# Optimization experiments

Hardware: AMD Instinct MI355X
Metric: run time of the kernel (lower is better)

The kernel has to match this reference:

```python
import jax, jax.numpy as jnp
import numpy as np
from jax import lax


def setup_inputs() -> dict:
    key = jax.random.key(0)
    k1, k2, k3, k4 = jax.random.split(key, 4)
    N, T = 4096, 64          # num_nodes, tokens per node
    V, H, L = 30000, 256, 2  # vocab, hidden size, LSTM layers
    data = jax.random.randint(k1, (N, T), 0, V, dtype=jnp.int64)
    embed = jax.random.uniform(k2, (V, H), jnp.float32, -0.1, 0.1)
    Wx = jax.random.normal(k3, (L, H, 4 * H), jnp.float32) * 0.05
    Wh = jax.random.normal(k4, (L, H, 4 * H), jnp.float32) * 0.05
    b = jnp.zeros((L, 4 * H), jnp.float32)
    return {"data": data, "embed": embed, "Wx": Wx, "Wh": Wh, "b": b}


def _stacked_lstm_last(tok, Wx, Wh, b):
    # tok: [N, T, H]; Wx/Wh: [L, H, 4H]; b: [L, 4H]
    L, H = Wx.shape[0], Wx.shape[1]
    N = tok.shape[0]
    xs = jnp.swapaxes(tok, 0, 1)  # [T, N, H] -- scan over time, batched over nodes
    c0 = jnp.zeros((L, N, H), tok.dtype)
    h0 = jnp.zeros((L, N, H), tok.dtype)

    def step(carry, x_t):
        c, h = carry
        inp = x_t
        new_c, new_h = [], []
        for l in range(L):  # small fixed layer loop
            z = inp @ Wx[l] + h[l] @ Wh[l] + b[l]  # [N, 4H]
            i, f, g, o = jnp.split(z, 4, axis=-1)   # flax gate order i, f, g, o
            i, f, o = jax.nn.sigmoid(i), jax.nn.sigmoid(f), jax.nn.sigmoid(o)
            g = jnp.tanh(g)
            cl = f * c[l] + i * g
            hl = o * jnp.tanh(cl)
            new_c.append(cl)
            new_h.append(hl)
            inp = hl  # top layer output feeds next layer
        return (jnp.stack(new_c), jnp.stack(new_h)), None

    (_, hF), _ = lax.scan(step, (c0, h0), xs)
    # result[-1] in the original is the top-layer output at the final step,
    # which equals the final top-layer hidden state.
    return hF[-1]  # [N, H]


def reference(data, embed, Wx, Wh, b):
    tok = embed[data]  # [N, T, H] embedding lookup
    return _stacked_lstm_last(tok, Wx, Wh, b)
```

## Files before the change

### kernel.cpp

```cpp
#include <hip/hip_runtime.h>
#include <hip/hip_bf16.h>

#define TT 64
#define HH 256
#define GG 1024

typedef _Float16 f16;
typedef __attribute__((ext_vector_type(8))) _Float16 f16x8;
typedef __attribute__((ext_vector_type(4))) _Float16 f16x4;
typedef __attribute__((ext_vector_type(4))) float f32x4;

__device__ __forceinline__ float sig_(float x) {
    return 1.0f / (1.0f + __expf(-x));
}
__device__ __forceinline__ float tanh_(float x) {
    x = fminf(fmaxf(x, -15.0f), 15.0f);
    float e = __expf(-2.0f * x);
    return (1.0f - e) / (1.0f + e);
}

__global__ void pack_weights(const float* __restrict__ Wx, const float* __restrict__ Wh,
                             f16* __restrict__ Wp) {
    int t = blockIdx.x * 256 + threadIdx.x;
    int lane = t & 63;
    int nt = (t >> 6) & 63;
    int kk = (t >> 12) & 15;
    int l = t >> 16;
    int n = nt * 16 + (lane & 15);
    int kbase = kk * 32 + 8 * (lane >> 4);
    const float* src = (kbase < 256) ? (Wx + (size_t)l * HH * GG + (size_t)kbase * GG + n)
                                     : (Wh + (size_t)l * HH * GG + (size_t)(kbase - 256) * GG + n);
    f16x8 v;
#pragma unroll
    for (int j = 0; j < 8; ++j) v[j] = (f16)src[(size_t)j * GG];
    *(f16x8*)(Wp + (size_t)t * 8) = v;
}

__global__ __launch_bounds__(512) void embw_gemm(
    const float* __restrict__ embed, const float* __restrict__ bias,
    const f16* __restrict__ Wp, f16* __restrict__ embW, int vocab)
{
    __shared__ f16 a_lds[32 * HH];
    const int tid = threadIdx.x;
    const int lane = tid & 63;
    const int w = tid >> 6;
    const int arow = lane & 15;
    const int g4 = lane >> 4;
    const int r0 = blockIdx.x * 32;

#pragma unroll
    for (int i = 0; i < 4; ++i) {
        int chunk = tid + i * 512;
        int row = chunk >> 6;
        int c4 = chunk & 63;
        int grow = r0 + row; if (grow >= vocab) grow = vocab - 1;
        float4 v = *(const float4*)(embed + (size_t)grow * HH + c4 * 4);
        int idx = row * HH + ((c4 * 4) ^ ((row & 7) << 3));
        *(f16x4*)&a_lds[idx] = (f16x4){(f16)v.x, (f16)v.y, (f16)v.z, (f16)v.w};
    }
    __syncthreads();

    float breg[8];
#pragma unroll
    for (int tt = 0; tt < 8; ++tt) breg[tt] = bias[(w * 8 + tt) * 16 + arow];

    f32x4 acc[2][8];
#pragma unroll
    for (int mt = 0; mt < 2; ++mt)
#pragma unroll
        for (int tt = 0; tt < 8; ++tt)
            acc[mt][tt] = (f32x4){breg[tt], breg[tt], breg[tt], breg[tt]};

    const f16* wl = Wp + (size_t)lane * 8;
#pragma unroll 2
    for (int kk = 0; kk < 8; ++kk) {
        int sw = (kk * 32 + g4 * 8) ^ ((arow & 7) << 3);
        f16x8 a0 = *(const f16x8*)&a_lds[arow * HH + sw];
        f16x8 a1 = *(const f16x8*)&a_lds[(arow + 16) * HH + sw];
        const f16* wkk = wl + (size_t)kk * 64 * 64 * 8;
#pragma unroll
        for (int tt = 0; tt < 8; ++tt) {
            f16x8 b = *(const f16x8*)(wkk + (size_t)(w * 8 + tt) * 64 * 8);
            acc[0][tt] = __builtin_amdgcn_mfma_f32_16x16x32_f16(a0, b, acc[0][tt], 0, 0, 0);
            acc[1][tt] = __builtin_amdgcn_mfma_f32_16x16x32_f16(a1, b, acc[1][tt], 0, 0, 0);
        }
    }

#pragma unroll
    for (int mt = 0; mt < 2; ++mt)
#pragma unroll
        for (int tt = 0; tt < 8; ++tt)
#pragma unroll
            for (int r = 0; r < 4; ++r) {
                int row = r0 + mt * 16 + g4 * 4 + r;
                if (row < vocab) {
                    int col = (w * 8 + tt) * 16 + arow;
                    embW[(size_t)row * GG + col] = (f16)acc[mt][tt][r];
                }
            }
}

#define NB2 16
#define LDZ 1032
#define LDH 264

__global__ __launch_bounds__(512, 2) void lstm_rec2(
    const int* __restrict__ data, const float* __restrict__ bias,
    const f16* __restrict__ embW, const f16* __restrict__ Wp,
    float* __restrict__ out)
{
    __shared__ f16 zx[NB2 * LDZ];
    __shared__ f16 h0s[NB2 * LDH];
    __shared__ f16 h1s[NB2 * LDH];

    const int tid = threadIdx.x;
    const int lane = tid & 63;
    const int w = tid >> 6;
    const int arow = lane & 15;
    const int g4 = lane >> 4;
    const int n0 = blockIdx.x * NB2;

    for (int i = tid; i < NB2 * LDH; i += 512) { h0s[i] = (f16)0; h1s[i] = (f16)0; }

    float breg1[8];
#pragma unroll
    for (int tt = 0; tt < 8; ++tt) {
        int col = (tt >> 1) * 256 + w * 32 + (tt & 1) * 16 + arow;
        breg1[tt] = bias[GG + col];
    }

    float c0[8], c1[8];
#pragma unroll
    for (int i = 0; i < 8; ++i) { c0[i] = 0.0f; c1[i] = 0.0f; }

    __syncthreads();

    const f16* wl0 = Wp + (size_t)8 * 64 * 64 * 8 + (size_t)lane * 8;
    const f16* wl1 = Wp + (size_t)16 * 64 * 64 * 8 + (size_t)lane * 8;

    for (int t = 0; t < TT; ++t) {
        {
            int n = tid >> 5;
            int cg = (tid & 31) * 32;
            int row = data[(n0 + n) * TT + t];
            const f16* src = embW + (size_t)row * GG + cg;
            f16x8 v0 = *(const f16x8*)src;
            f16x8 v1 = *(const f16x8*)(src + 8);
            f16x8 v2 = *(const f16x8*)(src + 16);
            f16x8 v3 = *(const f16x8*)(src + 24);
            f16* dst = &zx[n * LDZ + cg];
            *(f16x8*)dst = v0;
            *(f16x8*)(dst + 8) = v1;
            *(f16x8*)(dst + 16) = v2;
            *(f16x8*)(dst + 24) = v3;
        }
        __syncthreads();

        f32x4 acc[8];
#pragma unroll
        for (int tt = 0; tt < 8; ++tt) {
            int col = (tt >> 1) * 256 + w * 32 + (tt & 1) * 16 + arow;
#pragma unroll
            for (int r = 0; r < 4; ++r)
                acc[tt][r] = (float)zx[(g4 * 4 + r) * LDZ + col];
        }

#pragma unroll 2
        for (int kk = 0; kk < 8; ++kk) {
            int k0 = kk * 32 + 8 * g4;
            f16x8 a0 = *(const f16x8*)&h0s[arow * LDH + k0];
            const f16* wkk = wl0 + (size_t)kk * 64 * 64 * 8;
#pragma unroll
            for (int tt = 0; tt < 8; ++tt) {
                int nt = (tt >> 1) * 16 + w * 2 + (tt & 1);
                f16x8 b = *(const f16x8*)(wkk + (size_t)nt * 64 * 8);
                acc[tt] = __builtin_amdgcn_mfma_f32_16x16x32_f16(a0, b, acc[tt], 0, 0, 0);
            }
        }
        __syncthreads();

#pragma unroll
        for (int sub = 0; sub < 2; ++sub)
#pragma unroll
            for (int r = 0; r < 4; ++r) {
                int node = g4 * 4 + r;
                float i_ = sig_(acc[0 + sub][r]);
                float f_ = sig_(acc[2 + sub][r]);
                float g_ = tanh_(acc[4 + sub][r]);
                float o_ = sig_(acc[6 + sub][r]);
                int ci = sub * 4 + r;
                float c = fmaf(f_, c0[ci], i_ * g_);
                c0[ci] = c;
                int u = w * 32 + sub * 16 + arow;
                h0s[node * LDH + u] = (f16)(o_ * tanh_(c));
            }
        __syncthreads();

        f32x4 acc1[8];
#pragma unroll
        for (int tt = 0; tt < 8; ++tt)
            acc1[tt] = (f32x4){breg1[tt], breg1[tt], breg1[tt], breg1[tt]};

#pragma unroll 2
        for (int kk = 0; kk < 16; ++kk) {
            const f16* asrc = (kk < 8) ? h0s : h1s;
            int k0 = (kk & 7) * 32 + 8 * g4;
            f16x8 a0 = *(const f16x8*)&asrc[arow * LDH + k0];
            const f16* wkk = wl1 + (size_t)kk * 64 * 64 * 8;
#pragma unroll
            for (int tt = 0; tt < 8; ++tt) {
                int nt = (tt >> 1) * 16 + w * 2 + (tt & 1);
                f16x8 b = *(const f16x8*)(wkk + (size_t)nt * 64 * 8);
                acc1[tt] = __builtin_amdgcn_mfma_f32_16x16x32_f16(a0, b, acc1[tt], 0, 0, 0);
            }
        }
        __syncthreads();

#pragma unroll
        for (int sub = 0; sub < 2; ++sub)
#pragma unroll
            for (int r = 0; r < 4; ++r) {
                int node = g4 * 4 + r;
                float i_ = sig_(acc1[0 + sub][r]);
                float f_ = sig_(acc1[2 + sub][r]);
                float g_ = tanh_(acc1[4 + sub][r]);
                float o_ = sig_(acc1[6 + sub][r]);
                int ci = sub * 4 + r;
                float c = fmaf(f_, c1[ci], i_ * g_);
                c1[ci] = c;
                int u = w * 32 + sub * 16 + arow;
                h1s[node * LDH + u] = (f16)(o_ * tanh_(c));
            }
    }
    __syncthreads();

    for (int i = tid; i < NB2 * HH; i += 512) {
        int n = i >> 8, k = i & 255;
        out[(size_t)(n0 + n) * HH + k] = (float)h1s[n * LDH + k];
    }
}

__global__ void convert_embed(const float* __restrict__ e, f16* __restrict__ o, int n8) {
    int i = blockIdx.x * 256 + threadIdx.x;
    if (i >= n8) return;
    size_t p = (size_t)i * 8;
    float4 a = *(const float4*)(e + p);
    float4 b = *(const float4*)(e + p + 4);
    f16x8 v = { (f16)a.x, (f16)a.y, (f16)a.z, (f16)a.w,
                (f16)b.x, (f16)b.y, (f16)b.z, (f16)b.w };
    *(f16x8*)(o + p) = v;
}

#define FB 32
#define FTH 512
#define FLD 264
__device__ __forceinline__ void fb_layer_step(
    const f16 (*bx)[FLD], f16 (*bh)[FLD], const f16* __restrict__ wlayer,
    const float* breg_l, float* c_l, int lane, int w)
{
    f32x4 acc[2][8];
#pragma unroll
    for (int mt = 0; mt < 2; ++mt)
#pragma unroll
        for (int tt = 0; tt < 8; ++tt) {
            float b = breg_l[tt];
            acc[mt][tt] = (f32x4){b, b, b, b};
        }
    const int arow = lane & 15;
    const int koff = 8 * (lane >> 4);
    const f16* wl = wlayer + (size_t)lane * 8;
#pragma unroll 2
    for (int kk = 0; kk < 16; ++kk) {
        int k0 = (kk & 7) * 32 + koff;
        const f16(*src)[FLD] = (kk < 8) ? bx : (const f16(*)[FLD])bh;
        f16x8 a0 = *(const f16x8*)&src[arow][k0];
        f16x8 a1 = *(const f16x8*)&src[arow + 16][k0];
        const f16* wkk = wl + (size_t)kk * 64 * 64 * 8;
#pragma unroll
        for (int tt = 0; tt < 8; ++tt) {
            int nt = (tt >> 1) * 16 + w * 2 + (tt & 1);
            f16x8 b = *(const f16x8*)(wkk + (size_t)nt * 64 * 8);
            acc[0][tt] = __builtin_amdgcn_mfma_f32_16x16x32_f16(a0, b, acc[0][tt], 0, 0, 0);
            acc[1][tt] = __builtin_amdgcn_mfma_f32_16x16x32_f16(a1, b, acc[1][tt], 0, 0, 0);
        }
    }
    __syncthreads();
#pragma unroll
    for (int mt = 0; mt < 2; ++mt)
#pragma unroll
        for (int sub = 0; sub < 2; ++sub) {
            f32x4 iv = acc[mt][0 + sub], fv = acc[mt][2 + sub];
            f32x4 gv = acc[mt][4 + sub], ov = acc[mt][6 + sub];
#pragma unroll
            for (int r = 0; r < 4; ++r) {
                float i_ = sig_(iv[r]), f_ = sig_(fv[r]), g_ = tanh_(gv[r]), o_ = sig_(ov[r]);
                int ci = mt * 8 + sub * 4 + r;
                float c = fmaf(f_, c_l[ci], i_ * g_);
                c_l[ci] = c;
                int node = mt * 16 + (lane >> 4) * 4 + r;
                int unit = w * 32 + sub * 16 + (lane & 15);
                bh[node][unit] = (f16)(o_ * tanh_(c));
            }
        }
    __syncthreads();
}

__global__ __launch_bounds__(FTH, 2) void lstm_mfma_fb(
    const int* __restrict__ data, const float* __restrict__ bias,
    const f16* __restrict__ emb, const f16* __restrict__ Wp,
    float* __restrict__ out, int vocab)
{
    __shared__ f16 x_lds[FB][FLD];
    __shared__ f16 h0_lds[FB][FLD];
    __shared__ f16 h1_lds[FB][FLD];
    const int tid = threadIdx.x;
    const int lane = tid & 63;
    const int w = tid >> 6;
    const int n0 = blockIdx.x * FB;
    for (int i = tid; i < FB * FLD; i += FTH) {
        (&h0_lds[0][0])[i] = (f16)0.0f; (&h1_lds[0][0])[i] = (f16)0.0f;
    }
    float breg[2][8];
#pragma unroll
    for (int l = 0; l < 2; ++l)
#pragma unroll
        for (int tt = 0; tt < 8; ++tt) {
            int col = (tt >> 1) * 256 + w * 32 + (tt & 1) * 16 + (lane & 15);
            breg[l][tt] = bias[l * GG + col];
        }
    float cst[2][16];
#pragma unroll
    for (int i = 0; i < 32; ++i) (&cst[0][0])[i] = 0.0f;
    __syncthreads();
    const f16* Wp0 = Wp;
    const f16* Wp1 = Wp + (size_t)16 * 64 * 64 * 8;
    for (int t = 0; t < TT; ++t) {
        {
            int n = tid >> 4;
            int cg = (tid & 15) * 16;
            int row = data[(n0 + n) * TT + t];
            row = min(max(row, 0), vocab - 1);
            const f16* src = emb + (size_t)row * HH + cg;
            *(f16x8*)&x_lds[n][cg] = *(const f16x8*)src;
            *(f16x8*)&x_lds[n][cg + 8] = *(const f16x8*)(src + 8);
        }
        __syncthreads();
        fb_layer_step(x_lds, h0_lds, Wp0, breg[0], cst[0], lane, w);
        fb_layer_step((const f16(*)[FLD])h0_lds, h1_lds, Wp1, breg[1], cst[1], lane, w);
    }
    for (int i = tid; i < FB * HH; i += FTH) {
        int n = i >> 8, k = i & 255;
        out[(size_t)(n0 + n) * HH + k] = (float)h1_lds[n][k];
    }
}

extern "C" void kernel_launch(void* const* d_in, const int* in_sizes, int n_in,
                              void* d_out, int out_size, void* d_ws, size_t ws_size,
                              hipStream_t stream) {
    const int* data = (const int*)d_in[0];
    const float* embed = (const float*)d_in[1];
    const float* Wx = (const float*)d_in[2];
    const float* Wh = (const float*)d_in[3];
    const float* bias = (const float*)d_in[4];
    float* out = (float*)d_out;
    const int vocab = in_sizes[1] / HH;
    const int nNodes = in_sizes[0] / TT;

    const size_t wp_bytes = (size_t)2 * 16 * 64 * 64 * 8 * 2;
    const size_t embw_bytes = (size_t)vocab * GG * 2;
    const size_t emb16_bytes = (size_t)vocab * HH * 2;

    if (ws_size >= embw_bytes + wp_bytes) {
        f16* embW = (f16*)d_ws;
        f16* Wp = (f16*)((char*)d_ws + embw_bytes);
        pack_weights<<<dim3(512), dim3(256), 0, stream>>>(Wx, Wh, Wp);
        embw_gemm<<<dim3((vocab + 31) / 32), dim3(512), 0, stream>>>(embed, bias, Wp, embW, vocab);
        lstm_rec2<<<dim3(nNodes / NB2), dim3(512), 0, stream>>>(data, bias, embW, Wp, out);
        return;
    }
    f16* emb_h = (f16*)d_ws;
    f16* Wp = (f16*)((char*)d_ws + emb16_bytes);
    int n8 = in_sizes[1] / 8;
    convert_embed<<<dim3((n8 + 255) / 256), dim3(256), 0, stream>>>(embed, emb_h, n8);
    pack_weights<<<dim3(512), dim3(256), 0, stream>>>(Wx, Wh, Wp);
    lstm_mfma_fb<<<dim3(nNodes / FB), dim3(FTH), 0, stream>>>(data, bias, emb_h, Wp, out, vocab);
}
```

Measured before the change: 1.295 ms.

## Process 32 nodes per block in recurrent LSTM kernel and use fast exp2/rcp activations

Doubles the nodes per block in lstm_rec2 from 16 to 32, so each weight fragment loaded from global memory feeds two MFMAs (two M-tiles) instead of one. This halves the weight traffic per node for the recurrent matmuls. In exchange it uses more registers and shared memory and drops occupancy to one block per CU, with half as many blocks in the grid. The sigmoid and tanh helpers also switch to hardware exp2 and rcp intrinsics without clamping, while the fallback kernel keeps the precise versions.

```diff
diff --git a/kernel.cpp b/kernel.cpp
--- a/kernel.cpp
+++ b/kernel.cpp
@@ -10,10 +10,15 @@
 typedef __attribute__((ext_vector_type(4))) _Float16 f16x4;
 typedef __attribute__((ext_vector_type(4))) float f32x4;
 
+__device__ __forceinline__ float exp2_(float x) { return __builtin_amdgcn_exp2f(x); }
 __device__ __forceinline__ float sig_(float x) {
-    return 1.0f / (1.0f + __expf(-x));
+    return __builtin_amdgcn_rcpf(1.0f + exp2_(-1.44269504f * x));
 }
 __device__ __forceinline__ float tanh_(float x) {
+    return 1.0f - 2.0f * __builtin_amdgcn_rcpf(1.0f + exp2_(2.88539008f * x));
+}
+__device__ __forceinline__ float sigp_(float x) { return 1.0f / (1.0f + __expf(-x)); }
+__device__ __forceinline__ float tanhp_(float x) {
     x = fminf(fmaxf(x, -15.0f), 15.0f);
     float e = __expf(-2.0f * x);
     return (1.0f - e) / (1.0f + e);
@@ -100,11 +105,11 @@
             }
 }
 
-#define NB2 16
+#define NB2 32
 #define LDZ 1032
 #define LDH 264
 
-__global__ __launch_bounds__(512, 2) void lstm_rec2(
+__global__ __launch_bounds__(512, 1) void lstm_rec2(
     const int* __restrict__ data, const float* __restrict__ bias,
     const f16* __restrict__ embW, const f16* __restrict__ Wp,
     float* __restrict__ out)
@@ -120,6 +125,10 @@
     const int g4 = lane >> 4;
     const int n0 = blockIdx.x * NB2;
 
+    const int sn = tid >> 4;
+    const int scg = (tid & 15) * 64;
+    const int srow_base = (n0 + sn) * TT;
+
     for (int i = tid; i < NB2 * LDH; i += 512) { h0s[i] = (f16)0; h1s[i] = (f16)0; }
 
     float breg1[8];
@@ -129,108 +138,112 @@
         breg1[tt] = bias[GG + col];
     }
 
-    float c0[8], c1[8];
-#pragma unroll
-    for (int i = 0; i < 8; ++i) { c0[i] = 0.0f; c1[i] = 0.0f; }
-
-    __syncthreads();
+    float c0[16], c1[16];
+#pragma unroll
+    for (int i = 0; i < 16; ++i) { c0[i] = 0.0f; c1[i] = 0.0f; }
 
     const f16* wl0 = Wp + (size_t)8 * 64 * 64 * 8 + (size_t)lane * 8;
     const f16* wl1 = Wp + (size_t)16 * 64 * 64 * 8 + (size_t)lane * 8;
 
+#pragma unroll 1
     for (int t = 0; t < TT; ++t) {
         {
-            int n = tid >> 5;
-            int cg = (tid & 31) * 32;
-            int row = data[(n0 + n) * TT + t];
-            const f16* src = embW + (size_t)row * GG + cg;
-            f16x8 v0 = *(const f16x8*)src;
-            f16x8 v1 = *(const f16x8*)(src + 8);
-            f16x8 v2 = *(const f16x8*)(src + 16);
-            f16x8 v3 = *(const f16x8*)(src + 24);
-            f16* dst = &zx[n * LDZ + cg];
-            *(f16x8*)dst = v0;
-            *(f16x8*)(dst + 8) = v1;
-            *(f16x8*)(dst + 16) = v2;
-            *(f16x8*)(dst + 24) = v3;
+            int row = data[srow_base + t];
+            const f16* src = embW + (size_t)row * GG + scg;
+            f16* dst = &zx[sn * LDZ + scg];
+#pragma unroll
+            for (int j = 0; j < 8; ++j)
+                *(f16x8*)(dst + j * 8) = *(const f16x8*)(src + j * 8);
         }
         __syncthreads();
 
-        f32x4 acc[8];
-#pragma unroll
-        for (int tt = 0; tt < 8; ++tt) {
-            int col = (tt >> 1) * 256 + w * 32 + (tt & 1) * 16 + arow;
-#pragma unroll
-            for (int r = 0; r < 4; ++r)
-                acc[tt][r] = (float)zx[(g4 * 4 + r) * LDZ + col];
-        }
+        f32x4 acc[2][8];
+#pragma unroll
+        for (int mt = 0; mt < 2; ++mt)
+#pragma unroll
+            for (int tt = 0; tt < 8; ++tt) {
+                int col = (tt >> 1) * 256 + w * 32 + (tt & 1) * 16 + arow;
+#pragma unroll
+                for (int r = 0; r < 4; ++r)
+                    acc[mt][tt][r] = (float)zx[(mt * 16 + g4 * 4 + r) * LDZ + col];
+            }
 
 #pragma unroll 2
         for (int kk = 0; kk < 8; ++kk) {
             int k0 = kk * 32 + 8 * g4;
             f16x8 a0 = *(const f16x8*)&h0s[arow * LDH + k0];
+            f16x8 a1 = *(const f16x8*)&h0s[(arow + 16) * LDH + k0];
             const f16* wkk = wl0 + (size_t)kk * 64 * 64 * 8;
 #pragma unroll
             for (int tt = 0; tt < 8; ++tt) {
                 int nt = (tt >> 1) * 16 + w * 2 + (tt & 1);
                 f16x8 b = *(const f16x8*)(wkk + (size_t)nt * 64 * 8);
-                acc[tt] = __builtin_amdgcn_mfma_f32_16x16x32_f16(a0, b, acc[tt], 0, 0, 0);
+                acc[0][tt] = __builtin_amdgcn_mfma_f32_16x16x32_f16(a0, b, acc[0][tt], 0, 0, 0);
+                acc[1][tt] = __builtin_amdgcn_mfma_f32_16x16x32_f16(a1, b, acc[1][tt], 0, 0, 0);
             }
         }
         __syncthreads();
 
 #pragma unroll
-        for (int sub = 0; sub < 2; ++sub)
-#pragma unroll
-            for (int r = 0; r < 4; ++r) {
-                int node = g4 * 4 + r;
-                float i_ = sig_(acc[0 + sub][r]);
-                float f_ = sig_(acc[2 + sub][r]);
-                float g_ = tanh_(acc[4 + sub][r]);
-                float o_ = sig_(acc[6 + sub][r]);
-                int ci = sub * 4 + r;
-                float c = fmaf(f_, c0[ci], i_ * g_);
-                c0[ci] = c;
-                int u = w * 32 + sub * 16 + arow;
-                h0s[node * LDH + u] = (f16)(o_ * tanh_(c));
-            }
+        for (int mt = 0; mt < 2; ++mt)
+#pragma unroll
+            for (int sub = 0; sub < 2; ++sub)
+#pragma unroll
+                for (int r = 0; r < 4; ++r) {
+                    int node = mt * 16 + g4 * 4 + r;
+                    float i_ = sig_(acc[mt][0 + sub][r]);
+                    float f_ = sig_(acc[mt][2 + sub][r]);
+                    float g_ = tanh_(acc[mt][4 + sub][r]);
+                    float o_ = sig_(acc[mt][6 + sub][r]);
+                    int ci = mt * 8 + sub * 4 + r;
+                    float c = fmaf(f_, c0[ci], i_ * g_);
+                    c0[ci] = c;
+                    int u = w * 32 + sub * 16 + arow;
+                    h0s[node * LDH + u] = (f16)(o_ * tanh_(c));
+                }
         __syncthreads();
 
-        f32x4 acc1[8];
-#pragma unroll
-        for (int tt = 0; tt < 8; ++tt)
-            acc1[tt] = (f32x4){breg1[tt], breg1[tt], breg1[tt], breg1[tt]};
+        f32x4 acc1[2][8];
+#pragma unroll
+        for (int mt = 0; mt < 2; ++mt)
+#pragma unroll
+            for (int tt = 0; tt < 8; ++tt)
+                acc1[mt][tt] = (f32x4){breg1[tt], breg1[tt], breg1[tt], breg1[tt]};
 
 #pragma unroll 2
         for (int kk = 0; kk < 16; ++kk) {
             const f16* asrc = (kk < 8) ? h0s : h1s;
             int k0 = (kk & 7) * 32 + 8 * g4;
             f16x8 a0 = *(const f16x8*)&asrc[arow * LDH + k0];
+            f16x8 a1 = *(const f16x8*)&asrc[(arow + 16) * LDH + k0];
             const f16* wkk = wl1 + (size_t)kk * 64 * 64 * 8;
 #pragma unroll
             for (int tt = 0; tt < 8; ++tt) {
                 int nt = (tt >> 1) * 16 + w * 2 + (tt & 1);
                 f16x8 b = *(const f16x8*)(wkk + (size_t)nt * 64 * 8);
-                acc1[tt] = __builtin_amdgcn_mfma_f32_16x16x32_f16(a0, b, acc1[tt], 0, 0, 0);
+                acc1[0][tt] = __builtin_amdgcn_mfma_f32_16x16x32_f16(a0, b, acc1[0][tt], 0, 0, 0);
+                acc1[1][tt] = __builtin_amdgcn_mfma_f32_16x16x32_f16(a1, b, acc1[1][tt], 0, 0, 0);
             }
         }
         __syncthreads();
 
 #pragma unroll
-        for (int sub = 0; sub < 2; ++sub)
-#pragma unroll
-            for (int r = 0; r < 4; ++r) {
-                int node = g4 * 4 + r;
-                float i_ = sig_(acc1[0 + sub][r]);
-                float f_ = sig_(acc1[2 + sub][r]);
-                float g_ = tanh_(acc1[4 + sub][r]);
-                float o_ = sig_(acc1[6 + sub][r]);
-                int ci = sub * 4 + r;
-                float c = fmaf(f_, c1[ci], i_ * g_);
-                c1[ci] = c;
-                int u = w * 32 + sub * 16 + arow;
-                h1s[node * LDH + u] = (f16)(o_ * tanh_(c));
-            }
+        for (int mt = 0; mt < 2; ++mt)
+#pragma unroll
+            for (int sub = 0; sub < 2; ++sub)
+#pragma unroll
+                for (int r = 0; r < 4; ++r) {
+                    int node = mt * 16 + g4 * 4 + r;
+                    float i_ = sig_(acc1[mt][0 + sub][r]);
+                    float f_ = sig_(acc1[mt][2 + sub][r]);
+                    float g_ = tanh_(acc1[mt][4 + sub][r]);
+                    float o_ = sig_(acc1[mt][6 + sub][r]);
+                    int ci = mt * 8 + sub * 4 + r;
+                    float c = fmaf(f_, c1[ci], i_ * g_);
+                    c1[ci] = c;
+                    int u = w * 32 + sub * 16 + arow;
+                    h1s[node * LDH + u] = (f16)(o_ * tanh_(c));
+                }
     }
     __syncthreads();
 
@@ -293,13 +306,13 @@
             f32x4 gv = acc[mt][4 + sub], ov = acc[mt][6 + sub];
 #pragma unroll
             for (int r = 0; r < 4; ++r) {
-                float i_ = sig_(iv[r]), f_ = sig_(fv[r]), g_ = tanh_(gv[r]), o_ = sig_(ov[r]);
+                float i_ = sigp_(iv[r]), f_ = sigp_(fv[r]), g_ = tanhp_(gv[r]), o_ = sigp_(ov[r]);
                 int ci = mt * 8 + sub * 4 + r;
                 float c = fmaf(f_, c_l[ci], i_ * g_);
                 c_l[ci] = c;
                 int node = mt * 16 + (lane >> 4) * 4 + r;
                 int unit = w * 32 + sub * 16 + (lane & 15);
-                bh[node][unit] = (f16)(o_ * tanh_(c));
+                bh[node][unit] = (f16)(o_ * tanhp_(c));
             }
         }
     __syncthreads();
```

After: 1.228 ms. -5.2%, faster.
